# Performance work log

Hardware: AMD Instinct MI355X
Metric: run time of the kernel (lower is better)

The kernel has to match this reference:

```python
import jax, jax.numpy as jnp
import numpy as np

N_NODES = 100000
IN_DIM = 64
HIDDEN = 128
N_EDGES = 1600000


def sage_conv(x, src, dst, W_l, W_r, b):
    # PyG SAGEConv (mean aggr): out = lin_l(mean_{j in N(i)} x_j) + lin_r(x_i) + bias
    agg = jax.ops.segment_sum(x[src], dst, num_segments=N_NODES)  # [N, d]
    cnt = jax.ops.segment_sum(jnp.ones((src.shape[0],), x.dtype), dst,
                              num_segments=N_NODES)  # [N]
    mean = agg / jnp.maximum(cnt, 1.0)[:, None]
    return mean @ W_l + x @ W_r + b


def setup_inputs() -> dict:
    key = jax.random.key(0)
    ks = jax.random.split(key, 10)
    x = jax.random.normal(ks[0], (N_NODES, IN_DIM), dtype=jnp.float32)
    edge_index = jax.random.randint(ks[1], (2, N_EDGES), 0, N_NODES, dtype=jnp.int64)
    s = 1.0 / np.sqrt(IN_DIM)
    W_l1 = jax.random.uniform(ks[2], (IN_DIM, HIDDEN), jnp.float32, -s, s)
    W_r1 = jax.random.uniform(ks[3], (IN_DIM, HIDDEN), jnp.float32, -s, s)
    b1 = jnp.zeros((HIDDEN,), jnp.float32)
    s2 = 1.0 / np.sqrt(HIDDEN)
    W_l2 = jax.random.uniform(ks[4], (HIDDEN, HIDDEN), jnp.float32, -s2, s2)
    W_r2 = jax.random.uniform(ks[5], (HIDDEN, HIDDEN), jnp.float32, -s2, s2)
    b2 = jnp.zeros((HIDDEN,), jnp.float32)
    W_out = jax.random.uniform(ks[6], (HIDDEN, 1), jnp.float32, -s2, s2)
    b_out = jnp.zeros((1,), jnp.float32)
    return {"x": x, "edge_index": edge_index,
            "W_l1": W_l1, "W_r1": W_r1, "b1": b1,
            "W_l2": W_l2, "W_r2": W_r2, "b2": b2,
            "W_out": W_out, "b_out": b_out}


def reference(x, edge_index, W_l1, W_r1, b1, W_l2, W_r2, b2, W_out, b_out):
    src, dst = edge_index[0], edge_index[1]
    h1 = jax.nn.relu(sage_conv(x, src, dst, W_l1, W_r1, b1))   # [N, H]
    h2 = sage_conv(h1, src, dst, W_l2, W_r2, b2)               # [N, H]
    out = (h2 @ W_out + b_out).squeeze(-1)                     # [N]
    return out, h1, h2
```

## Files before the change

### kernel.cpp

```cpp
#include <hip/hip_runtime.h>

#define NN 100000
#define IND 64
#define HID 128
#define NE 1600000

#define BKT2 256
#define NBKT2 ((NN + BKT2 - 1) / BKT2)
#define CAP 4992
#define EPB 4096
#define NBLK_E ((NE + EPB - 1) / EPB)

#define SCAN_CHUNK 1024
#define NSB ((NN + SCAN_CHUNK - 1) / SCAN_CHUNK)

typedef __attribute__((ext_vector_type(8))) short bf16x8;
typedef __attribute__((ext_vector_type(4))) float f32x4;
typedef __attribute__((ext_vector_type(2))) float f32x2;

static __device__ __forceinline__ unsigned short f2bf(float f) {
    unsigned u = __float_as_uint(f);
    u = (u + 0x7FFFu + ((u >> 16) & 1u)) >> 16;
    return (unsigned short)u;
}
static __device__ __forceinline__ unsigned pack2(float a, float b) {
    return (unsigned)f2bf(a) | ((unsigned)f2bf(b) << 16);
}


__global__ __launch_bounds__(512) void zero_small_kernel(int* __restrict__ p, int n) {
    int i = threadIdx.x;
    if (i < n) p[i] = 0;
}

__global__ __launch_bounds__(512) void binA_kernel(const int* __restrict__ src,
                                                   const int* __restrict__ dst,
                                                   int* __restrict__ bktcur,
                                                   unsigned* __restrict__ bins) {
    __shared__ int hcnt[NBKT2];
    __shared__ int rbase[NBKT2];
    int t = threadIdx.x;
    int e0 = blockIdx.x * EPB;
    int ce = min(EPB, NE - e0);
    for (int i = t; i < NBKT2; i += 512) hcnt[i] = 0;
    __syncthreads();
    for (int i = t; i < ce; i += 512)
        atomicAdd(&hcnt[dst[e0 + i] >> 8], 1);
    __syncthreads();
    for (int i = t; i < NBKT2; i += 512) {
        int c = hcnt[i];
        rbase[i] = c ? atomicAdd(&bktcur[i], c) : 0;
        hcnt[i] = 0;
    }
    __syncthreads();
    for (int i = t; i < ce; i += 512) {
        int d = dst[e0 + i];
        int b = d >> 8;
        int r = atomicAdd(&hcnt[b], 1);
        bins[(size_t)b * CAP + rbase[b] + r] =
            (unsigned)src[e0 + i] | ((unsigned)(d & 255) << 17);
    }
}

__global__ __launch_bounds__(256) void binB_kernel(const int* __restrict__ bktcur,
                                                   unsigned* __restrict__ bins,
                                                   int* __restrict__ cnt,
                                                   int* __restrict__ off) {
    __shared__ unsigned ebuf[CAP];
    __shared__ int ncnt[BKT2];
    __shared__ int nofs[BKT2];
    __shared__ int wtot[4];
    int t = threadIdx.x, lane = t & 63, w = t >> 6;
    int b = blockIdx.x;
    int m = bktcur[b];
    size_t base = (size_t)b * CAP;
    for (int i = t; i < m; i += 256) ebuf[i] = bins[base + i];
    ncnt[t] = 0;
    __syncthreads();
    for (int i = t; i < m; i += 256)
        atomicAdd(&ncnt[ebuf[i] >> 17], 1);
    __syncthreads();
    int v = ncnt[t];
    int incl = v;
    #pragma unroll
    for (int o = 1; o < 64; o <<= 1) {
        int u = __shfl_up(incl, o);
        if (lane >= o) incl += u;
    }
    if (lane == 63) wtot[w] = incl;
    __syncthreads();
    int wbase = 0;
    #pragma unroll
    for (int i = 0; i < 4; ++i) if (i < w) wbase += wtot[i];
    int ex = wbase + incl - v;
    nofs[t] = ex;
    int node = b * BKT2 + t;
    if (node < NN) { cnt[node] = v; off[node] = (int)base + ex; }
    __syncthreads();
    for (int i = t; i < m; i += 256) {
        unsigned val = ebuf[i];
        int r = atomicAdd(&nofs[val >> 17], 1);
        bins[base + r] = val & 0x1FFFFu;
    }
}


__global__ __launch_bounds__(256) void cvt_xq_kernel(const float4* __restrict__ x,
                                                     unsigned* __restrict__ xq) {
    int i = blockIdx.x * 256 + threadIdx.x;
    float4 v = x[i];
    int u = __builtin_amdgcn_cvt_pk_fp8_f32(v.x, v.y, 0, false);
    u = __builtin_amdgcn_cvt_pk_fp8_f32(v.z, v.w, u, true);
    xq[i] = (unsigned)u;
}

__global__ __launch_bounds__(256) void packW_kernel(const float* __restrict__ Wr,
                                                    const float* __restrict__ Wl,
                                                    int Khalf, int KS,
                                                    unsigned short* __restrict__ Wp) {
    int t = blockIdx.x * 256 + threadIdx.x;
    if (t >= 8 * KS * 64) return;
    int l  = t & 63;
    int ks = (t >> 6) % KS;
    int jt = t / (64 * KS);
    int j  = jt * 16 + (l & 15);
    int kb = ks * 32 + (l >> 4) * 8;
    unsigned short v[8];
    #pragma unroll
    for (int i = 0; i < 8; ++i) {
        int k = kb + i;
        float w = (k < Khalf) ? Wr[k * HID + j] : Wl[(k - Khalf) * HID + j];
        v[i] = f2bf(w);
    }
    ushort4 lo, hi;
    lo.x = v[0]; lo.y = v[1]; lo.z = v[2]; lo.w = v[3];
    hi.x = v[4]; hi.y = v[5]; hi.z = v[6]; hi.w = v[7];
    ushort4* d = reinterpret_cast<ushort4*>(Wp + (size_t)t * 8);
    d[0] = lo; d[1] = hi;
}


__global__ __launch_bounds__(256) void agg1_kernel(const unsigned char* __restrict__ xq,
                                                   const int* __restrict__ srcs,
                                                   const int* __restrict__ off,
                                                   const int* __restrict__ cnt,
                                                   unsigned short* __restrict__ m1b) {
    int t = threadIdx.x;
    int n = blockIdx.x * 4 + (t >> 6);
    int l = t & 63, ep = l >> 4, d4 = (l & 15) * 4;
    int s0 = off[n], deg = cnt[n];
    float a0 = 0.f, a1 = 0.f, a2 = 0.f, a3 = 0.f;
    int e = ep;
    for (; e + 4 < deg; e += 8) {
        int sA = srcs[s0 + e], sB = srcs[s0 + e + 4];
        unsigned uA = *reinterpret_cast<const unsigned*>(xq + (size_t)sA * IND + d4);
        unsigned uB = *reinterpret_cast<const unsigned*>(xq + (size_t)sB * IND + d4);
        f32x2 lA = __builtin_amdgcn_cvt_pk_f32_fp8((int)uA, false);
        f32x2 hA = __builtin_amdgcn_cvt_pk_f32_fp8((int)uA, true);
        f32x2 lB = __builtin_amdgcn_cvt_pk_f32_fp8((int)uB, false);
        f32x2 hB = __builtin_amdgcn_cvt_pk_f32_fp8((int)uB, true);
        a0 += lA.x + lB.x; a1 += lA.y + lB.y;
        a2 += hA.x + hB.x; a3 += hA.y + hB.y;
    }
    for (; e < deg; e += 4) {
        int s = srcs[s0 + e];
        unsigned u = *reinterpret_cast<const unsigned*>(xq + (size_t)s * IND + d4);
        f32x2 lo = __builtin_amdgcn_cvt_pk_f32_fp8((int)u, false);
        f32x2 hi = __builtin_amdgcn_cvt_pk_f32_fp8((int)u, true);
        a0 += lo.x; a1 += lo.y; a2 += hi.x; a3 += hi.y;
    }
    a0 += __shfl_down(a0, 32); a1 += __shfl_down(a1, 32);
    a2 += __shfl_down(a2, 32); a3 += __shfl_down(a3, 32);
    a0 += __shfl_down(a0, 16); a1 += __shfl_down(a1, 16);
    a2 += __shfl_down(a2, 16); a3 += __shfl_down(a3, 16);
    if (l < 16) {
        float inv = 1.f / fmaxf((float)deg, 1.f);
        uint2 o;
        o.x = pack2(a0 * inv, a1 * inv);
        o.y = pack2(a2 * inv, a3 * inv);
        *reinterpret_cast<uint2*>(m1b + (size_t)n * IND + d4) = o;
    }
}

__global__ __launch_bounds__(256) void agg2_kernel(const unsigned char* __restrict__ h1q,
                                                   const int* __restrict__ srcs,
                                                   const int* __restrict__ off,
                                                   const int* __restrict__ cnt,
                                                   unsigned short* __restrict__ m2b) {
    int t = threadIdx.x;
    int n = blockIdx.x * 4 + (t >> 6);
    int l = t & 63, ep = l >> 5, d4 = (l & 31) * 4;
    int s0 = off[n], deg = cnt[n];
    float a0 = 0.f, a1 = 0.f, a2 = 0.f, a3 = 0.f;
    int e = ep;
    for (; e + 6 < deg; e += 8) {
        int sA = srcs[s0 + e],     sB = srcs[s0 + e + 2];
        int sC = srcs[s0 + e + 4], sD = srcs[s0 + e + 6];
        unsigned uA = *reinterpret_cast<const unsigned*>(h1q + (size_t)sA * HID + d4);
        unsigned uB = *reinterpret_cast<const unsigned*>(h1q + (size_t)sB * HID + d4);
        unsigned uC = *reinterpret_cast<const unsigned*>(h1q + (size_t)sC * HID + d4);
        unsigned uD = *reinterpret_cast<const unsigned*>(h1q + (size_t)sD * HID + d4);
        f32x2 lA = __builtin_amdgcn_cvt_pk_f32_fp8((int)uA, false);
        f32x2 hA = __builtin_amdgcn_cvt_pk_f32_fp8((int)uA, true);
        f32x2 lB = __builtin_amdgcn_cvt_pk_f32_fp8((int)uB, false);
        f32x2 hB = __builtin_amdgcn_cvt_pk_f32_fp8((int)uB, true);
        f32x2 lC = __builtin_amdgcn_cvt_pk_f32_fp8((int)uC, false);
        f32x2 hC = __builtin_amdgcn_cvt_pk_f32_fp8((int)uC, true);
        f32x2 lD = __builtin_amdgcn_cvt_pk_f32_fp8((int)uD, false);
        f32x2 hD = __builtin_amdgcn_cvt_pk_f32_fp8((int)uD, true);
        a0 += (lA.x + lB.x) + (lC.x + lD.x);
        a1 += (lA.y + lB.y) + (lC.y + lD.y);
        a2 += (hA.x + hB.x) + (hC.x + hD.x);
        a3 += (hA.y + hB.y) + (hC.y + hD.y);
    }
    for (; e < deg; e += 2) {
        int s = srcs[s0 + e];
        unsigned u = *reinterpret_cast<const unsigned*>(h1q + (size_t)s * HID + d4);
        f32x2 lo = __builtin_amdgcn_cvt_pk_f32_fp8((int)u, false);
        f32x2 hi = __builtin_amdgcn_cvt_pk_f32_fp8((int)u, true);
        a0 += lo.x; a1 += lo.y; a2 += hi.x; a3 += hi.y;
    }
    a0 += __shfl_down(a0, 32); a1 += __shfl_down(a1, 32);
    a2 += __shfl_down(a2, 32); a3 += __shfl_down(a3, 32);
    if (l < 32) {
        float inv = 1.f / fmaxf((float)deg, 1.f);
        uint2 o;
        o.x = pack2(a0 * inv, a1 * inv);
        o.y = pack2(a2 * inv, a3 * inv);
        *reinterpret_cast<uint2*>(m2b + (size_t)n * HID + d4) = o;
    }
}


__global__ __launch_bounds__(256) void mfma1_kernel(const float* __restrict__ x,
                                                    const unsigned short* __restrict__ m1b,
                                                    const unsigned short* __restrict__ Wp,
                                                    const float* __restrict__ b,
                                                    float* __restrict__ h1f,
                                                    unsigned short* __restrict__ h1b,
                                                    unsigned char* __restrict__ h1q) {
    int t = threadIdx.x, w = t >> 6, l = t & 63;
    int row0 = blockIdx.x * 64 + w * 16;
    int arow = row0 + (l & 15); if (arow > NN - 1) arow = NN - 1;
    int kcol = (l >> 4) * 8;
    f32x4 acc[8];
    #pragma unroll
    for (int jt = 0; jt < 8; ++jt) { acc[jt][0] = 0.f; acc[jt][1] = 0.f; acc[jt][2] = 0.f; acc[jt][3] = 0.f; }
    #pragma unroll
    for (int ks = 0; ks < 4; ++ks) {
        bf16x8 a;
        int c = (ks & 1) * 32 + kcol;
        if (ks < 2) {
            const float* xr = x + (size_t)arow * IND + c;
            float4 f0 = *reinterpret_cast<const float4*>(xr);
            float4 f1 = *reinterpret_cast<const float4*>(xr + 4);
            a[0] = (short)f2bf(f0.x); a[1] = (short)f2bf(f0.y);
            a[2] = (short)f2bf(f0.z); a[3] = (short)f2bf(f0.w);
            a[4] = (short)f2bf(f1.x); a[5] = (short)f2bf(f1.y);
            a[6] = (short)f2bf(f1.z); a[7] = (short)f2bf(f1.w);
        } else {
            a = *reinterpret_cast<const bf16x8*>(m1b + (size_t)arow * IND + c);
        }
        #pragma unroll
        for (int jt = 0; jt < 8; ++jt) {
            bf16x8 bb = *reinterpret_cast<const bf16x8*>(Wp + ((size_t)(jt * 4 + ks) * 64 + l) * 8);
            acc[jt] = __builtin_amdgcn_mfma_f32_16x16x32_bf16(a, bb, acc[jt], 0, 0, 0);
        }
    }
    int rbase = row0 + (l >> 4) * 4;
    #pragma unroll
    for (int jt = 0; jt < 8; ++jt) {
        int col = jt * 16 + (l & 15);
        float bias = b[col];
        #pragma unroll
        for (int r = 0; r < 4; ++r) {
            int row = rbase + r;
            if (row < NN) {
                float v = fmaxf(acc[jt][r] + bias, 0.f);
                h1f[(size_t)row * HID + col] = v;
                h1b[(size_t)row * HID + col] = f2bf(v);
                unsigned q8 = (unsigned)__builtin_amdgcn_cvt_pk_fp8_f32(v, 0.f, 0, false) & 0xFFu;
                h1q[(size_t)row * HID + col] = (unsigned char)q8;
            }
        }
    }
}

__global__ __launch_bounds__(256) void mfma2_kernel(const unsigned short* __restrict__ h1b,
                                                    const unsigned short* __restrict__ m2b,
                                                    const unsigned short* __restrict__ Wp,
                                                    const float* __restrict__ b,
                                                    const float* __restrict__ Wout,
                                                    const float* __restrict__ bout,
                                                    float* __restrict__ h2f,
                                                    float* __restrict__ out) {
    int t = threadIdx.x, w = t >> 6, l = t & 63;
    int row0 = blockIdx.x * 64 + w * 16;
    int arow = row0 + (l & 15); if (arow > NN - 1) arow = NN - 1;
    int kcol = (l >> 4) * 8;
    f32x4 acc[8];
    #pragma unroll
    for (int jt = 0; jt < 8; ++jt) { acc[jt][0] = 0.f; acc[jt][1] = 0.f; acc[jt][2] = 0.f; acc[jt][3] = 0.f; }
    #pragma unroll
    for (int ks = 0; ks < 8; ++ks) {
        const unsigned short* A = (ks < 4) ? h1b : m2b;
        int c = (ks & 3) * 32 + kcol;
        bf16x8 a = *reinterpret_cast<const bf16x8*>(A + (size_t)arow * HID + c);
        #pragma unroll
        for (int jt = 0; jt < 8; ++jt) {
            bf16x8 bb = *reinterpret_cast<const bf16x8*>(Wp + ((size_t)(jt * 8 + ks) * 64 + l) * 8);
            acc[jt] = __builtin_amdgcn_mfma_f32_16x16x32_bf16(a, bb, acc[jt], 0, 0, 0);
        }
    }
    int rbase = row0 + (l >> 4) * 4;
    float hs0 = 0.f, hs1 = 0.f, hs2 = 0.f, hs3 = 0.f;
    #pragma unroll
    for (int jt = 0; jt < 8; ++jt) {
        int col = jt * 16 + (l & 15);
        float bias = b[col];
        float wo = Wout[col];
        #pragma unroll
        for (int r = 0; r < 4; ++r) {
            int row = rbase + r;
            float v = acc[jt][r] + bias;
            if (row < NN) h2f[(size_t)row * HID + col] = v;
            if (r == 0) hs0 += v * wo;
            else if (r == 1) hs1 += v * wo;
            else if (r == 2) hs2 += v * wo;
            else hs3 += v * wo;
        }
    }
    #pragma unroll
    for (int o = 1; o < 16; o <<= 1) {
        hs0 += __shfl_xor(hs0, o);
        hs1 += __shfl_xor(hs1, o);
        hs2 += __shfl_xor(hs2, o);
        hs3 += __shfl_xor(hs3, o);
    }
    if ((l & 15) == 0) {
        float bo = bout[0];
        if (rbase + 0 < NN) out[rbase + 0] = hs0 + bo;
        if (rbase + 1 < NN) out[rbase + 1] = hs1 + bo;
        if (rbase + 2 < NN) out[rbase + 2] = hs2 + bo;
        if (rbase + 3 < NN) out[rbase + 3] = hs3 + bo;
    }
}


__global__ __launch_bounds__(256) void zero_int_kernel(int4* __restrict__ p, int n4) {
    int i = blockIdx.x * 256 + threadIdx.x;
    if (i < n4) p[i] = make_int4(0, 0, 0, 0);
}

__global__ __launch_bounds__(256) void hist_kernel(const int* __restrict__ dst,
                                                   int* __restrict__ cnt) {
    int e = blockIdx.x * 256 + threadIdx.x;
    if (e < NE) atomicAdd(&cnt[dst[e]], 1);
}

__global__ __launch_bounds__(256) void scanA_kernel(const int* __restrict__ cnt,
                                                    int* __restrict__ bsums) {
    int b = blockIdx.x, t = threadIdx.x;
    int base = b * SCAN_CHUNK + t * 4;
    int s = 0;
    #pragma unroll
    for (int k = 0; k < 4; ++k) { int i = base + k; if (i < NN) s += cnt[i]; }
    #pragma unroll
    for (int o = 32; o > 0; o >>= 1) s += __shfl_down(s, o);
    __shared__ int wsum[4];
    if ((t & 63) == 0) wsum[t >> 6] = s;
    __syncthreads();
    if (t == 0) bsums[b] = wsum[0] + wsum[1] + wsum[2] + wsum[3];
}

__global__ void scanB_kernel(int* __restrict__ bsums) {
    int acc = 0;
    for (int i = 0; i < NSB; ++i) { int v = bsums[i]; bsums[i] = acc; acc += v; }
}

__global__ __launch_bounds__(256) void scanC_kernel(const int* __restrict__ cnt,
                                                    const int* __restrict__ bsums,
                                                    int* __restrict__ off,
                                                    int* __restrict__ cur) {
    int b = blockIdx.x, t = threadIdx.x;
    int lane = t & 63, w = t >> 6;
    int base = b * SCAN_CHUNK + t * 4;
    int v[4]; int s = 0;
    #pragma unroll
    for (int k = 0; k < 4; ++k) {
        int i = base + k;
        v[k] = (i < NN) ? cnt[i] : 0;
        s += v[k];
    }
    int inc = s;
    #pragma unroll
    for (int o = 1; o < 64; o <<= 1) {
        int xv = __shfl_up(inc, o);
        if (lane >= o) inc += xv;
    }
    __shared__ int wsum[4];
    if (lane == 63) wsum[w] = inc;
    __syncthreads();
    int wbase = 0;
    for (int i = 0; i < w; ++i) wbase += wsum[i];
    int ex = bsums[b] + wbase + (inc - s);
    #pragma unroll
    for (int k = 0; k < 4; ++k) {
        int i = base + k;
        if (i < NN) { off[i] = ex; cur[i] = ex; }
        ex += v[k];
    }
}

__global__ __launch_bounds__(256) void fill_kernel(const int* __restrict__ src,
                                                   const int* __restrict__ dst,
                                                   int* __restrict__ cur,
                                                   int* __restrict__ srcs) {
    int e = blockIdx.x * 256 + threadIdx.x;
    if (e < NE) {
        int p = atomicAdd(&cur[dst[e]], 1);
        srcs[p] = src[e];
    }
}

__global__ __launch_bounds__(256) void agg1f_kernel(const float* __restrict__ x,
                                                    const int* __restrict__ srcs,
                                                    const int* __restrict__ off,
                                                    const int* __restrict__ cnt,
                                                    float* __restrict__ mean1) {
    int t = threadIdx.x;
    int n = blockIdx.x * 4 + (t >> 6);
    int d = t & 63;
    int s0 = off[n], deg = cnt[n];
    float acc = 0.f;
    for (int e = 0; e < deg; ++e) acc += x[(size_t)srcs[s0 + e] * IND + d];
    mean1[(size_t)n * HID + d] = acc / fmaxf((float)deg, 1.f);
}

__global__ __launch_bounds__(256) void agg2f_kernel(const float* __restrict__ h1,
                                                    const int* __restrict__ srcs,
                                                    const int* __restrict__ off,
                                                    const int* __restrict__ cnt,
                                                    float* __restrict__ mean2) {
    int t = threadIdx.x;
    int n = blockIdx.x * 2 + (t >> 7);
    int d = t & 127;
    int s0 = off[n], deg = cnt[n];
    float acc = 0.f;
    for (int e = 0; e < deg; ++e) acc += h1[(size_t)srcs[s0 + e] * HID + d];
    mean2[(size_t)n * HID + d] = acc / fmaxf((float)deg, 1.f);
}

__global__ __launch_bounds__(256) void gemm1f_kernel(const float* __restrict__ x,
                                                     const float* __restrict__ Wl,
                                                     const float* __restrict__ Wr,
                                                     const float* __restrict__ b,
                                                     float* __restrict__ h1) {
    __shared__ float in[16][128];
    int t = threadIdx.x;
    int node0 = blockIdx.x * 16;
    for (int idx = t; idx < 16 * 128; idx += 256) {
        int r = idx >> 7, c = idx & 127;
        in[r][c] = (c < IND) ? x[(size_t)(node0 + r) * IND + c]
                             : h1[(size_t)(node0 + r) * HID + (c - IND)];
    }
    __syncthreads();
    int j = t & 127, g = t >> 7;
    float acc[8];
    float bj = b[j];
    #pragma unroll
    for (int q = 0; q < 8; ++q) acc[q] = bj;
    for (int k = 0; k < 128; ++k) {
        float wv = (k < IND) ? Wr[k * HID + j] : Wl[(k - IND) * HID + j];
        #pragma unroll
        for (int q = 0; q < 8; ++q) acc[q] += in[g * 8 + q][k] * wv;
    }
    #pragma unroll
    for (int q = 0; q < 8; ++q)
        h1[(size_t)(node0 + g * 8 + q) * HID + j] = fmaxf(acc[q], 0.f);
}

__global__ __launch_bounds__(256) void gemm2f_kernel(const float* __restrict__ h1,
                                                     const float* __restrict__ Wl,
                                                     const float* __restrict__ Wr,
                                                     const float* __restrict__ b,
                                                     const float* __restrict__ Wout,
                                                     const float* __restrict__ bout,
                                                     float* __restrict__ h2,
                                                     float* __restrict__ out) {
    __shared__ float in[16][256];
    __shared__ float part[4][8];
    int t = threadIdx.x;
    int node0 = blockIdx.x * 16;
    for (int idx = t; idx < 16 * 256; idx += 256) {
        int r = idx >> 8, c = idx & 255;
        in[r][c] = (c < HID) ? h1[(size_t)(node0 + r) * HID + c]
                             : h2[(size_t)(node0 + r) * HID + (c - HID)];
    }
    __syncthreads();
    int j = t & 127, g = t >> 7, lane = t & 63, w = t >> 6;
    float acc[8];
    float bj = b[j];
    #pragma unroll
    for (int q = 0; q < 8; ++q) acc[q] = bj;
    for (int k = 0; k < 256; ++k) {
        float wv = (k < HID) ? Wr[k * HID + j] : Wl[(k - HID) * HID + j];
        #pragma unroll
        for (int q = 0; q < 8; ++q) acc[q] += in[g * 8 + q][k] * wv;
    }
    float wo = Wout[j];
    #pragma unroll
    for (int q = 0; q < 8; ++q)
        h2[(size_t)(node0 + g * 8 + q) * HID + j] = acc[q];
    #pragma unroll
    for (int q = 0; q < 8; ++q) {
        float v = acc[q] * wo;
        #pragma unroll
        for (int o = 32; o > 0; o >>= 1) v += __shfl_down(v, o);
        if (lane == 0) part[w][q] = v;
    }
    __syncthreads();
    if (t < 16) {
        int gg = t >> 3, q = t & 7;
        out[node0 + t] = part[2 * gg][q] + part[2 * gg + 1][q] + bout[0];
    }
}


extern "C" void kernel_launch(void* const* d_in, const int* in_sizes, int n_in,
                              void* d_out, int out_size, void* d_ws, size_t ws_size,
                              hipStream_t stream) {
    const float* x    = (const float*)d_in[0];
    const int*   eidx = (const int*)d_in[1];
    const int*   src  = eidx;
    const int*   dst  = eidx + NE;
    const float* Wl1  = (const float*)d_in[2];
    const float* Wr1  = (const float*)d_in[3];
    const float* b1   = (const float*)d_in[4];
    const float* Wl2  = (const float*)d_in[5];
    const float* Wr2  = (const float*)d_in[6];
    const float* b2   = (const float*)d_in[7];
    const float* Wout = (const float*)d_in[8];
    const float* bout = (const float*)d_in[9];

    float* out = (float*)d_out;
    float* h1f = out + NN;
    float* h2f = h1f + (size_t)NN * HID;

    char* p = (char*)d_ws;
    int* cnt        = (int*)p;            p += (size_t)NN * 4;
    int* off        = (int*)p;            p += (size_t)NN * 4;
    int* bktcur     = (int*)p;            p += 512 * 4;
    unsigned* bins  = (unsigned*)p;       p += (size_t)NBKT2 * CAP * 4;
    unsigned char* xq  = (unsigned char*)p;  p += (size_t)NN * IND;
    unsigned short* m1b = (unsigned short*)p; p += (size_t)NN * IND * 2;
    unsigned short* h1b = (unsigned short*)p; p += (size_t)NN * HID * 2;
    unsigned char* h1q  = (unsigned char*)p;  p += (size_t)NN * HID;
    unsigned short* m2b = (unsigned short*)p; p += (size_t)NN * HID * 2;
    unsigned short* Wp1 = (unsigned short*)p; p += 8 * 4 * 64 * 8 * 2;
    unsigned short* Wp2 = (unsigned short*)p; p += 8 * 8 * 64 * 8 * 2;
    const size_t need_v3 = (size_t)(p - (char*)d_ws);
    const size_t need_csr = ((size_t)3 * NN + 128 + NE) * sizeof(int);

    if (ws_size >= need_v3) {
        zero_small_kernel<<<1, 512, 0, stream>>>(bktcur, NBKT2);
        binA_kernel<<<NBLK_E, 512, 0, stream>>>(src, dst, bktcur, bins);
        binB_kernel<<<NBKT2, 256, 0, stream>>>(bktcur, bins, cnt, off);
        cvt_xq_kernel<<<(NN * IND / 4) / 256, 256, 0, stream>>>((const float4*)x, (unsigned*)xq);
        packW_kernel<<<8, 256, 0, stream>>>(Wr1, Wl1, IND, 4, Wp1);
        packW_kernel<<<16, 256, 0, stream>>>(Wr2, Wl2, HID, 8, Wp2);
        agg1_kernel<<<NN / 4, 256, 0, stream>>>(xq, (const int*)bins, off, cnt, m1b);
        mfma1_kernel<<<(NN + 63) / 64, 256, 0, stream>>>(x, m1b, Wp1, b1, h1f, h1b, h1q);
        agg2_kernel<<<NN / 4, 256, 0, stream>>>(h1q, (const int*)bins, off, cnt, m2b);
        mfma2_kernel<<<(NN + 63) / 64, 256, 0, stream>>>(h1b, m2b, Wp2, b2, Wout, bout, h2f, out);
    } else if (ws_size >= need_csr) {
        int* cntF   = (int*)d_ws;
        int* offF   = cntF + NN;
        int* curF   = offF + NN;
        int* bsums  = curF + NN;
        int* srcsF  = bsums + 128;
        zero_int_kernel<<<(NN / 4 + 255) / 256, 256, 0, stream>>>((int4*)cntF, NN / 4);
        hist_kernel<<<(NE + 255) / 256, 256, 0, stream>>>(dst, cntF);
        scanA_kernel<<<NSB, 256, 0, stream>>>(cntF, bsums);
        scanB_kernel<<<1, 1, 0, stream>>>(bsums);
        scanC_kernel<<<NSB, 256, 0, stream>>>(cntF, bsums, offF, curF);
        fill_kernel<<<(NE + 255) / 256, 256, 0, stream>>>(src, dst, curF, srcsF);
        agg1f_kernel<<<NN / 4, 256, 0, stream>>>(x, srcsF, offF, cntF, h1f);
        gemm1f_kernel<<<NN / 16, 256, 0, stream>>>(x, Wl1, Wr1, b1, h1f);
        agg2f_kernel<<<NN / 2, 256, 0, stream>>>(h1f, srcsF, offF, cntF, h2f);
        gemm2f_kernel<<<NN / 16, 256, 0, stream>>>(h1f, Wl2, Wr2, b2, Wout, bout, h2f, out);
    }
}
```

Baseline: 225.4 us.

## Fuse neighbor aggregation into MFMA GEMM kernels via shared-memory mean tiles

Merges each layer's gather-mean aggregation kernel into its MFMA GEMM kernel. The bf16 mean rows now stay in LDS and never round-trip through global memory. The bf16 copy of h1 is also dropped; layer 2 reads fp32 h1 and converts it on the fly. This removes two launches and several intermediate buffer writes and reads. In exchange, each block walks 64 nodes' neighbor lists serially per wave (16 nodes per wave), which lowers gather parallelism and latency hiding compared with one node per wave across many blocks.

```diff
diff --git a/kernel.cpp b/kernel.cpp
--- a/kernel.cpp
+++ b/kernel.cpp
@@ -140,107 +140,60 @@
 }
 
 
-__global__ __launch_bounds__(256) void agg1_kernel(const unsigned char* __restrict__ xq,
-                                                   const int* __restrict__ srcs,
-                                                   const int* __restrict__ off,
-                                                   const int* __restrict__ cnt,
-                                                   unsigned short* __restrict__ m1b) {
-    int t = threadIdx.x;
-    int n = blockIdx.x * 4 + (t >> 6);
-    int l = t & 63, ep = l >> 4, d4 = (l & 15) * 4;
-    int s0 = off[n], deg = cnt[n];
-    float a0 = 0.f, a1 = 0.f, a2 = 0.f, a3 = 0.f;
-    int e = ep;
-    for (; e + 4 < deg; e += 8) {
-        int sA = srcs[s0 + e], sB = srcs[s0 + e + 4];
-        unsigned uA = *reinterpret_cast<const unsigned*>(xq + (size_t)sA * IND + d4);
-        unsigned uB = *reinterpret_cast<const unsigned*>(xq + (size_t)sB * IND + d4);
-        f32x2 lA = __builtin_amdgcn_cvt_pk_f32_fp8((int)uA, false);
-        f32x2 hA = __builtin_amdgcn_cvt_pk_f32_fp8((int)uA, true);
-        f32x2 lB = __builtin_amdgcn_cvt_pk_f32_fp8((int)uB, false);
-        f32x2 hB = __builtin_amdgcn_cvt_pk_f32_fp8((int)uB, true);
-        a0 += lA.x + lB.x; a1 += lA.y + lB.y;
-        a2 += hA.x + hB.x; a3 += hA.y + hB.y;
-    }
-    for (; e < deg; e += 4) {
-        int s = srcs[s0 + e];
-        unsigned u = *reinterpret_cast<const unsigned*>(xq + (size_t)s * IND + d4);
-        f32x2 lo = __builtin_amdgcn_cvt_pk_f32_fp8((int)u, false);
-        f32x2 hi = __builtin_amdgcn_cvt_pk_f32_fp8((int)u, true);
-        a0 += lo.x; a1 += lo.y; a2 += hi.x; a3 += hi.y;
-    }
-    a0 += __shfl_down(a0, 32); a1 += __shfl_down(a1, 32);
-    a2 += __shfl_down(a2, 32); a3 += __shfl_down(a3, 32);
-    a0 += __shfl_down(a0, 16); a1 += __shfl_down(a1, 16);
-    a2 += __shfl_down(a2, 16); a3 += __shfl_down(a3, 16);
-    if (l < 16) {
-        float inv = 1.f / fmaxf((float)deg, 1.f);
-        uint2 o;
-        o.x = pack2(a0 * inv, a1 * inv);
-        o.y = pack2(a2 * inv, a3 * inv);
-        *reinterpret_cast<uint2*>(m1b + (size_t)n * IND + d4) = o;
-    }
-}
-
-__global__ __launch_bounds__(256) void agg2_kernel(const unsigned char* __restrict__ h1q,
-                                                   const int* __restrict__ srcs,
-                                                   const int* __restrict__ off,
-                                                   const int* __restrict__ cnt,
-                                                   unsigned short* __restrict__ m2b) {
-    int t = threadIdx.x;
-    int n = blockIdx.x * 4 + (t >> 6);
-    int l = t & 63, ep = l >> 5, d4 = (l & 31) * 4;
-    int s0 = off[n], deg = cnt[n];
-    float a0 = 0.f, a1 = 0.f, a2 = 0.f, a3 = 0.f;
-    int e = ep;
-    for (; e + 6 < deg; e += 8) {
-        int sA = srcs[s0 + e],     sB = srcs[s0 + e + 2];
-        int sC = srcs[s0 + e + 4], sD = srcs[s0 + e + 6];
-        unsigned uA = *reinterpret_cast<const unsigned*>(h1q + (size_t)sA * HID + d4);
-        unsigned uB = *reinterpret_cast<const unsigned*>(h1q + (size_t)sB * HID + d4);
-        unsigned uC = *reinterpret_cast<const unsigned*>(h1q + (size_t)sC * HID + d4);
-        unsigned uD = *reinterpret_cast<const unsigned*>(h1q + (size_t)sD * HID + d4);
-        f32x2 lA = __builtin_amdgcn_cvt_pk_f32_fp8((int)uA, false);
-        f32x2 hA = __builtin_amdgcn_cvt_pk_f32_fp8((int)uA, true);
-        f32x2 lB = __builtin_amdgcn_cvt_pk_f32_fp8((int)uB, false);
-        f32x2 hB = __builtin_amdgcn_cvt_pk_f32_fp8((int)uB, true);
-        f32x2 lC = __builtin_amdgcn_cvt_pk_f32_fp8((int)uC, false);
-        f32x2 hC = __builtin_amdgcn_cvt_pk_f32_fp8((int)uC, true);
-        f32x2 lD = __builtin_amdgcn_cvt_pk_f32_fp8((int)uD, false);
-        f32x2 hD = __builtin_amdgcn_cvt_pk_f32_fp8((int)uD, true);
-        a0 += (lA.x + lB.x) + (lC.x + lD.x);
-        a1 += (lA.y + lB.y) + (lC.y + lD.y);
-        a2 += (hA.x + hB.x) + (hC.x + hD.x);
-        a3 += (hA.y + hB.y) + (hC.y + hD.y);
-    }
-    for (; e < deg; e += 2) {
-        int s = srcs[s0 + e];
-        unsigned u = *reinterpret_cast<const unsigned*>(h1q + (size_t)s * HID + d4);
-        f32x2 lo = __builtin_amdgcn_cvt_pk_f32_fp8((int)u, false);
-        f32x2 hi = __builtin_amdgcn_cvt_pk_f32_fp8((int)u, true);
-        a0 += lo.x; a1 += lo.y; a2 += hi.x; a3 += hi.y;
-    }
-    a0 += __shfl_down(a0, 32); a1 += __shfl_down(a1, 32);
-    a2 += __shfl_down(a2, 32); a3 += __shfl_down(a3, 32);
-    if (l < 32) {
-        float inv = 1.f / fmaxf((float)deg, 1.f);
-        uint2 o;
-        o.x = pack2(a0 * inv, a1 * inv);
-        o.y = pack2(a2 * inv, a3 * inv);
-        *reinterpret_cast<uint2*>(m2b + (size_t)n * HID + d4) = o;
-    }
-}
-
-
-__global__ __launch_bounds__(256) void mfma1_kernel(const float* __restrict__ x,
-                                                    const unsigned short* __restrict__ m1b,
-                                                    const unsigned short* __restrict__ Wp,
-                                                    const float* __restrict__ b,
-                                                    float* __restrict__ h1f,
-                                                    unsigned short* __restrict__ h1b,
-                                                    unsigned char* __restrict__ h1q) {
+__global__ __launch_bounds__(256) void fused1_kernel(const float* __restrict__ x,
+                                                     const unsigned char* __restrict__ xq,
+                                                     const int* __restrict__ srcs,
+                                                     const int* __restrict__ off,
+                                                     const int* __restrict__ cnt,
+                                                     const unsigned short* __restrict__ Wp,
+                                                     const float* __restrict__ b,
+                                                     float* __restrict__ h1f,
+                                                     unsigned char* __restrict__ h1q) {
+    __shared__ unsigned short m1[64][IND + 8];
     int t = threadIdx.x, w = t >> 6, l = t & 63;
-    int row0 = blockIdx.x * 64 + w * 16;
+    int blk = blockIdx.x;
+    {
+        int ep = l >> 4, d4 = (l & 15) * 4;
+        for (int nn = 0; nn < 16; ++nn) {
+            int lr = w * 16 + nn;
+            int n = blk * 64 + lr;
+            int deg = (n < NN) ? cnt[n] : 0;
+            int s0 = (n < NN) ? off[n] : 0;
+            float a0 = 0.f, a1 = 0.f, a2 = 0.f, a3 = 0.f;
+            int e = ep;
+            for (; e + 4 < deg; e += 8) {
+                int sA = srcs[s0 + e], sB = srcs[s0 + e + 4];
+                unsigned uA = *reinterpret_cast<const unsigned*>(xq + (size_t)sA * IND + d4);
+                unsigned uB = *reinterpret_cast<const unsigned*>(xq + (size_t)sB * IND + d4);
+                f32x2 lA = __builtin_amdgcn_cvt_pk_f32_fp8((int)uA, false);
+                f32x2 hA = __builtin_amdgcn_cvt_pk_f32_fp8((int)uA, true);
+                f32x2 lB = __builtin_amdgcn_cvt_pk_f32_fp8((int)uB, false);
+                f32x2 hB = __builtin_amdgcn_cvt_pk_f32_fp8((int)uB, true);
+                a0 += lA.x + lB.x; a1 += lA.y + lB.y;
+                a2 += hA.x + hB.x; a3 += hA.y + hB.y;
+            }
+            for (; e < deg; e += 4) {
+                int s = srcs[s0 + e];
+                unsigned u = *reinterpret_cast<const unsigned*>(xq + (size_t)s * IND + d4);
+                f32x2 lo = __builtin_amdgcn_cvt_pk_f32_fp8((int)u, false);
+                f32x2 hi = __builtin_amdgcn_cvt_pk_f32_fp8((int)u, true);
+                a0 += lo.x; a1 += lo.y; a2 += hi.x; a3 += hi.y;
+            }
+            a0 += __shfl_down(a0, 32); a1 += __shfl_down(a1, 32);
+            a2 += __shfl_down(a2, 32); a3 += __shfl_down(a3, 32);
+            a0 += __shfl_down(a0, 16); a1 += __shfl_down(a1, 16);
+            a2 += __shfl_down(a2, 16); a3 += __shfl_down(a3, 16);
+            if (l < 16) {
+                float inv = 1.f / fmaxf((float)deg, 1.f);
+                uint2 o;
+                o.x = pack2(a0 * inv, a1 * inv);
+                o.y = pack2(a2 * inv, a3 * inv);
+                *reinterpret_cast<uint2*>(&m1[lr][d4]) = o;
+            }
+        }
+    }
+    __syncthreads();
+    int row0 = blk * 64 + w * 16;
     int arow = row0 + (l & 15); if (arow > NN - 1) arow = NN - 1;
     int kcol = (l >> 4) * 8;
     f32x4 acc[8];
@@ -259,7 +212,7 @@
             a[4] = (short)f2bf(f1.x); a[5] = (short)f2bf(f1.y);
             a[6] = (short)f2bf(f1.z); a[7] = (short)f2bf(f1.w);
         } else {
-            a = *reinterpret_cast<const bf16x8*>(m1b + (size_t)arow * IND + c);
+            a = *reinterpret_cast<const bf16x8*>(&m1[w * 16 + (l & 15)][c]);
         }
         #pragma unroll
         for (int jt = 0; jt < 8; ++jt) {
@@ -278,7 +231,6 @@
             if (row < NN) {
                 float v = fmaxf(acc[jt][r] + bias, 0.f);
                 h1f[(size_t)row * HID + col] = v;
-                h1b[(size_t)row * HID + col] = f2bf(v);
                 unsigned q8 = (unsigned)__builtin_amdgcn_cvt_pk_fp8_f32(v, 0.f, 0, false) & 0xFFu;
                 h1q[(size_t)row * HID + col] = (unsigned char)q8;
             }
@@ -286,16 +238,70 @@
     }
 }
 
-__global__ __launch_bounds__(256) void mfma2_kernel(const unsigned short* __restrict__ h1b,
-                                                    const unsigned short* __restrict__ m2b,
-                                                    const unsigned short* __restrict__ Wp,
-                                                    const float* __restrict__ b,
-                                                    const float* __restrict__ Wout,
-                                                    const float* __restrict__ bout,
-                                                    float* __restrict__ h2f,
-                                                    float* __restrict__ out) {
+
+__global__ __launch_bounds__(256) void fused2_kernel(const float* __restrict__ h1f,
+                                                     const unsigned char* __restrict__ h1q,
+                                                     const int* __restrict__ srcs,
+                                                     const int* __restrict__ off,
+                                                     const int* __restrict__ cnt,
+                                                     const unsigned short* __restrict__ Wp,
+                                                     const float* __restrict__ b,
+                                                     const float* __restrict__ Wout,
+                                                     const float* __restrict__ bout,
+                                                     float* __restrict__ h2f,
+                                                     float* __restrict__ out) {
+    __shared__ unsigned short m2[64][HID + 8];
     int t = threadIdx.x, w = t >> 6, l = t & 63;
-    int row0 = blockIdx.x * 64 + w * 16;
+    int blk = blockIdx.x;
+    {
+        int ep = l >> 5, d4 = (l & 31) * 4;
+        for (int nn = 0; nn < 16; ++nn) {
+            int lr = w * 16 + nn;
+            int n = blk * 64 + lr;
+            int deg = (n < NN) ? cnt[n] : 0;
+            int s0 = (n < NN) ? off[n] : 0;
+            float a0 = 0.f, a1 = 0.f, a2 = 0.f, a3 = 0.f;
+            int e = ep;
+            for (; e + 6 < deg; e += 8) {
+                int sA = srcs[s0 + e],     sB = srcs[s0 + e + 2];
+                int sC = srcs[s0 + e + 4], sD = srcs[s0 + e + 6];
+                unsigned uA = *reinterpret_cast<const unsigned*>(h1q + (size_t)sA * HID + d4);
+                unsigned uB = *reinterpret_cast<const unsigned*>(h1q + (size_t)sB * HID + d4);
+                unsigned uC = *reinterpret_cast<const unsigned*>(h1q + (size_t)sC * HID + d4);
+                unsigned uD = *reinterpret_cast<const unsigned*>(h1q + (size_t)sD * HID + d4);
+                f32x2 lA = __builtin_amdgcn_cvt_pk_f32_fp8((int)uA, false);
+                f32x2 hA = __builtin_amdgcn_cvt_pk_f32_fp8((int)uA, true);
+                f32x2 lB = __builtin_amdgcn_cvt_pk_f32_fp8((int)uB, false);
+                f32x2 hB = __builtin_amdgcn_cvt_pk_f32_fp8((int)uB, true);
+                f32x2 lC = __builtin_amdgcn_cvt_pk_f32_fp8((int)uC, false);
+                f32x2 hC = __builtin_amdgcn_cvt_pk_f32_fp8((int)uC, true);
+                f32x2 lD = __builtin_amdgcn_cvt_pk_f32_fp8((int)uD, false);
+                f32x2 hD = __builtin_amdgcn_cvt_pk_f32_fp8((int)uD, true);
+                a0 += (lA.x + lB.x) + (lC.x + lD.x);
+                a1 += (lA.y + lB.y) + (lC.y + lD.y);
+                a2 += (hA.x + hB.x) + (hC.x + hD.x);
+                a3 += (hA.y + hB.y) + (hC.y + hD.y);
+            }
+            for (; e < deg; e += 2) {
+                int s = srcs[s0 + e];
+                unsigned u = *reinterpret_cast<const unsigned*>(h1q + (size_t)s * HID + d4);
+                f32x2 lo = __builtin_amdgcn_cvt_pk_f32_fp8((int)u, false);
+                f32x2 hi = __builtin_amdgcn_cvt_pk_f32_fp8((int)u, true);
+                a0 += lo.x; a1 += lo.y; a2 += hi.x; a3 += hi.y;
+            }
+            a0 += __shfl_down(a0, 32); a1 += __shfl_down(a1, 32);
+            a2 += __shfl_down(a2, 32); a3 += __shfl_down(a3, 32);
+            if (l < 32) {
+                float inv = 1.f / fmaxf((float)deg, 1.f);
+                uint2 o;
+                o.x = pack2(a0 * inv, a1 * inv);
+                o.y = pack2(a2 * inv, a3 * inv);
+                *reinterpret_cast<uint2*>(&m2[lr][d4]) = o;
+            }
+        }
+    }
+    __syncthreads();
+    int row0 = blk * 64 + w * 16;
     int arow = row0 + (l & 15); if (arow > NN - 1) arow = NN - 1;
     int kcol = (l >> 4) * 8;
     f32x4 acc[8];
@@ -303,9 +309,19 @@
     for (int jt = 0; jt < 8; ++jt) { acc[jt][0] = 0.f; acc[jt][1] = 0.f; acc[jt][2] = 0.f; acc[jt][3] = 0.f; }
     #pragma unroll
     for (int ks = 0; ks < 8; ++ks) {
-        const unsigned short* A = (ks < 4) ? h1b : m2b;
+        bf16x8 a;
         int c = (ks & 3) * 32 + kcol;
-        bf16x8 a = *reinterpret_cast<const bf16x8*>(A + (size_t)arow * HID + c);
+        if (ks < 4) {
+            const float* hr = h1f + (size_t)arow * HID + c;
+            float4 f0 = *reinterpret_cast<const float4*>(hr);
+            float4 f1 = *reinterpret_cast<const float4*>(hr + 4);
+            a[0] = (short)f2bf(f0.x); a[1] = (short)f2bf(f0.y);
+            a[2] = (short)f2bf(f0.z); a[3] = (short)f2bf(f0.w);
+            a[4] = (short)f2bf(f1.x); a[5] = (short)f2bf(f1.y);
+            a[6] = (short)f2bf(f1.z); a[7] = (short)f2bf(f1.w);
+        } else {
+            a = *reinterpret_cast<const bf16x8*>(&m2[w * 16 + (l & 15)][c]);
+        }
         #pragma unroll
         for (int jt = 0; jt < 8; ++jt) {
             bf16x8 bb = *reinterpret_cast<const bf16x8*>(Wp + ((size_t)(jt * 8 + ks) * 64 + l) * 8);
@@ -552,27 +568,24 @@
     int* off        = (int*)p;            p += (size_t)NN * 4;
     int* bktcur     = (int*)p;            p += 512 * 4;
     unsigned* bins  = (unsigned*)p;       p += (size_t)NBKT2 * CAP * 4;
-    unsigned char* xq  = (unsigned char*)p;  p += (size_t)NN * IND;
-    unsigned short* m1b = (unsigned short*)p; p += (size_t)NN * IND * 2;
-    unsigned short* h1b = (unsigned short*)p; p += (size_t)NN * HID * 2;
-    unsigned char* h1q  = (unsigned char*)p;  p += (size_t)NN * HID;
-    unsigned short* m2b = (unsigned short*)p; p += (size_t)NN * HID * 2;
+    unsigned char* xq  = (unsigned char*)p;   p += (size_t)NN * IND;
+    unsigned char* h1q = (unsigned char*)p;   p += (size_t)NN * HID;
     unsigned short* Wp1 = (unsigned short*)p; p += 8 * 4 * 64 * 8 * 2;
     unsigned short* Wp2 = (unsigned short*)p; p += 8 * 8 * 64 * 8 * 2;
-    const size_t need_v3 = (size_t)(p - (char*)d_ws);
+    const size_t need_v4 = (size_t)(p - (char*)d_ws);
     const size_t need_csr = ((size_t)3 * NN + 128 + NE) * sizeof(int);
 
-    if (ws_size >= need_v3) {
+    if (ws_size >= need_v4) {
         zero_small_kernel<<<1, 512, 0, stream>>>(bktcur, NBKT2);
         binA_kernel<<<NBLK_E, 512, 0, stream>>>(src, dst, bktcur, bins);
         binB_kernel<<<NBKT2, 256, 0, stream>>>(bktcur, bins, cnt, off);
         cvt_xq_kernel<<<(NN * IND / 4) / 256, 256, 0, stream>>>((const float4*)x, (unsigned*)xq);
         packW_kernel<<<8, 256, 0, stream>>>(Wr1, Wl1, IND, 4, Wp1);
         packW_kernel<<<16, 256, 0, stream>>>(Wr2, Wl2, HID, 8, Wp2);
-        agg1_kernel<<<NN / 4, 256, 0, stream>>>(xq, (const int*)bins, off, cnt, m1b);
-        mfma1_kernel<<<(NN + 63) / 64, 256, 0, stream>>>(x, m1b, Wp1, b1, h1f, h1b, h1q);
-        agg2_kernel<<<NN / 4, 256, 0, stream>>>(h1q, (const int*)bins, off, cnt, m2b);
-        mfma2_kernel<<<(NN + 63) / 64, 256, 0, stream>>>(h1b, m2b, Wp2, b2, Wout, bout, h2f, out);
+        fused1_kernel<<<(NN + 63) / 64, 256, 0, stream>>>(x, xq, (const int*)bins, off, cnt,
+                                                          Wp1, b1, h1f, h1q);
+        fused2_kernel<<<(NN + 63) / 64, 256, 0, stream>>>(h1f, h1q, (const int*)bins, off, cnt,
+                                                          Wp2, b2, Wout, bout, h2f, out);
     } else if (ws_size >= need_csr) {
         int* cntF   = (int*)d_ws;
         int* offF   = cntF + NN;
```

After: 299.0 us. 32.6% more time.
